# Kernel tuning notes

Measured on AMD Instinct MI355X. Metric: run time of the kernel, lower is better.

The kernel has to match this reference:

```python
import jax, jax.numpy as jnp
import numpy as np

EMBED = 1024
HEADS = 16
HDIM = EMBED // HEADS  # k_dim == v_dim == 64
MAXPOS = 256
L = 2 * MAXPOS  # rpe table length = 512
B, S = 1, 2048
EPS = 1e-6


def setup_inputs() -> dict:
    key = jax.random.key(0)
    ks = jax.random.split(key, 16)
    def xavier(k, shape):
        fan_in, fan_out = shape[1], shape[0]
        std = (2.0 / (fan_in + fan_out)) ** 0.5
        return jax.random.normal(k, shape, dtype=jnp.float32) * std
    inp = {
        "query": jax.random.normal(ks[0], (B, S, EMBED), dtype=jnp.float32),
        "key":   jax.random.normal(ks[1], (B, S, EMBED), dtype=jnp.float32),
        "value": jax.random.normal(ks[2], (B, S, EMBED), dtype=jnp.float32),
        "pos":   jax.random.randint(ks[3], (B, S, S), 0, L, dtype=jnp.int32),
        "mask":  jnp.ones((B, S, S), dtype=jnp.float32),
        # projections (stored as [out, in] like torch Linear)
        "Wq": xavier(ks[4], (HEADS * HDIM, EMBED)), "bq": jnp.zeros((HEADS * HDIM,), jnp.float32),
        "Wk": xavier(ks[5], (HEADS * HDIM, EMBED)), "bk": jnp.zeros((HEADS * HDIM,), jnp.float32),
        "Wv": xavier(ks[6], (HEADS * HDIM, EMBED)), "bv": jnp.zeros((HEADS * HDIM,), jnp.float32),
        "rpe": jnp.zeros((L, HEADS, HDIM), jnp.float32) + 0.02 * jax.random.normal(ks[7], (L, HEADS, HDIM), dtype=jnp.float32),
        "Wqt": xavier(ks[8], (EMBED, EMBED)), "bqt": jnp.zeros((EMBED,), jnp.float32),
        "Wo": xavier(ks[9], (EMBED, HEADS * HDIM)), "bo": jnp.zeros((EMBED,), jnp.float32),
        "gamma": jnp.ones((EMBED,), jnp.float32),
        "beta": jnp.zeros((EMBED,), jnp.float32),
    }
    return inp


def _layer_norm(x, gamma, beta):
    mu = jnp.mean(x, axis=-1, keepdims=True)
    var = jnp.mean(jnp.square(x - mu), axis=-1, keepdims=True)
    return (x - mu) * jax.lax.rsqrt(var + EPS) * gamma + beta


def reference(query, key, value, pos, mask, Wq, bq, Wk, bk, Wv, bv, rpe, Wqt, bqt, Wo, bo, gamma, beta):
    b, s, _ = query.shape
    scaling = HDIM ** (-0.5)
    q = (query @ Wq.T + bq) * scaling          # [b,s,n*d]
    k = key @ Wk.T + bk
    v = value @ Wv.T + bv
    q = q.reshape(b, s, HEADS, HDIM)
    k = k.reshape(b, s, HEADS, HDIM)
    v = v.reshape(b, s, HEADS, HDIM)
    attn = jnp.einsum('bqnd,bknd->bqkn', q, k)          # [b,q,k,n]
    qrpe = jnp.einsum('bqnd,lnd->bqln', q, rpe)         # [b,q,L,n]
    idx = jnp.broadcast_to(pos[..., None], (b, s, s, HEADS))
    qrpe_g = jnp.take_along_axis(qrpe, idx, axis=2)     # gather per (q,k) pair
    attn = attn + qrpe_g
    attn = attn - (1.0 - mask[..., None]) * 1e6
    attn = jax.nn.softmax(attn, axis=-2)                # softmax over key axis
    out = jnp.einsum('bqkn,bknd->bqnd', attn, v).reshape(b, s, HEADS * HDIM)
    out = (out @ Wo.T + bo) + (query @ Wqt.T + bqt)
    return _layer_norm(out, gamma, beta)
```

## Files before the change

kernel.cpp:

```cpp
#include <hip/hip_runtime.h>


typedef short          bf16x8 __attribute__((ext_vector_type(8)));
typedef float          f32x4  __attribute__((ext_vector_type(4)));
typedef int            i32x4  __attribute__((ext_vector_type(4)));
typedef unsigned short u16x4  __attribute__((ext_vector_type(4)));
typedef unsigned short u16x8  __attribute__((ext_vector_type(8)));

#define SEQ 2048
#define EMB 1024
#define NH  16
#define HD  64
#define RL  512

#define MFMA16(a,b,c) __builtin_amdgcn_mfma_f32_16x16x32_bf16((a),(b),(c),0,0,0)

__device__ __forceinline__ unsigned short f2bf(float f){
  union{float f; unsigned u;} x; x.f=f;
  unsigned r = x.u + 0x7FFFu + ((x.u>>16)&1u);
  return (unsigned short)(r>>16);
}
__device__ __forceinline__ float bf2f(unsigned short u){
  union{unsigned u; float f;} x; x.u=((unsigned)u)<<16; return x.f;
}
__device__ __forceinline__ unsigned char f2e5(float f){
  union{_Float16 h; unsigned short u;} cv; cv.h = (_Float16)f;
  unsigned short b = cv.u;
  unsigned r = (unsigned)b + 0x7Fu + ((b>>8)&1u);
  return (unsigned char)(r>>8);
}
__device__ __forceinline__ float e52f(unsigned char b){
  union{unsigned short u; _Float16 h;} cv; cv.u = ((unsigned short)b)<<8;
  return (float)cv.h;
}
__device__ __forceinline__ void gload16(const void* g, void* l){
  __builtin_amdgcn_global_load_lds((const __attribute__((address_space(1))) unsigned int*)g,
                                   (__attribute__((address_space(3))) unsigned int*)l, 16, 0, 0);
}
__device__ __forceinline__ bf16x8 fragld(const unsigned short* t, int row, int chunk){
  int swz = chunk ^ (row & 7);
  return *(const bf16x8*)(t + row*64 + swz*8);
}

__global__ __launch_bounds__(256) void cvt_all(
    const float* __restrict__ s0, const float* __restrict__ s1, const float* __restrict__ s2,
    const float* __restrict__ s3, const float* __restrict__ s4, const float* __restrict__ s5,
    const float* __restrict__ s6, const float* __restrict__ s7,
    unsigned short* __restrict__ d0, unsigned short* __restrict__ d1, unsigned short* __restrict__ d2,
    unsigned short* __restrict__ d3, unsigned short* __restrict__ d4, unsigned short* __restrict__ d5,
    unsigned short* __restrict__ d6, unsigned short* __restrict__ d7)
{
  const float* s; unsigned short* d; int n;
  switch (blockIdx.y) {
    case 0: s=s0; d=d0; n=SEQ*EMB; break;
    case 1: s=s1; d=d1; n=SEQ*EMB; break;
    case 2: s=s2; d=d2; n=SEQ*EMB; break;
    case 3: s=s3; d=d3; n=EMB*EMB; break;
    case 4: s=s4; d=d4; n=EMB*EMB; break;
    case 5: s=s5; d=d5; n=EMB*EMB; break;
    case 6: s=s6; d=d6; n=EMB*EMB; break;
    default: s=s7; d=d7; n=EMB*EMB; break;
  }
  int i = (blockIdx.x*256 + threadIdx.x)*8;
  if (i >= n) return;
  f32x4 a = *(const f32x4*)(s+i);
  f32x4 b = *(const f32x4*)(s+i+4);
  u16x8 o;
  #pragma unroll
  for (int j=0;j<4;++j){ o[j]=f2bf(a[j]); o[4+j]=f2bf(b[j]); }
  *(u16x8*)(d+i) = o;
}

__global__ __launch_bounds__(256) void rpe_cvt(const float* __restrict__ src,
                                               unsigned short* __restrict__ dst)
{
  int i = (blockIdx.x*256 + threadIdx.x)*4;
  int l = i >> 10;
  int h = (i >> 6) & 15;
  int d = i & 63;
  f32x4 a = *(const f32x4*)(src + i);
  u16x4 o;
  #pragma unroll
  for (int j=0;j<4;++j) o[j]=f2bf(a[j]);
  *(u16x4*)(dst + ((size_t)h*RL + l)*HD + d) = o;
}

__global__ __launch_bounds__(256) void pack_pm(const int* __restrict__ pos,
                                               const float* __restrict__ mask,
                                               unsigned short* __restrict__ pm)
{
  int i = (blockIdx.x*256 + threadIdx.x)*4;
  i32x4 p = *(const i32x4*)(pos + i);
  f32x4 m = *(const f32x4*)(mask + i);
  u16x4 o;
  #pragma unroll
  for (int j=0;j<4;++j) o[j] = (m[j] > 0.5f) ? (unsigned short)p[j] : (unsigned short)512;
  *(u16x4*)(pm + i) = o;
}

__device__ __forceinline__ void gemm_core(const unsigned short* __restrict__ A,
                                          const unsigned short* __restrict__ W,
                                          unsigned short* At, unsigned short* Wt,
                                          f32x4 acc[4][4], int m0, int n0)
{
  const int tid = threadIdx.x, lane = tid & 63, w = tid >> 6;
  const int rg = lane >> 3, sc = (lane & 7) ^ rg;
  const int c = lane & 15, g = lane >> 4;
  const int wm = w >> 1, wn = w & 1;

  for (int kt = 0; kt < EMB/64; ++kt) {
    __syncthreads();
    #pragma unroll
    for (int i = 0; i < 4; ++i) {
      int r = w*32 + i*8 + rg;
      gload16(A + (size_t)(m0+r)*EMB + kt*64 + sc*8, At + (w*32 + i*8)*64);
      gload16(W + (size_t)(n0+r)*EMB + kt*64 + sc*8, Wt + (w*32 + i*8)*64);
    }
    __syncthreads();
    #pragma unroll
    for (int kk = 0; kk < 2; ++kk) {
      bf16x8 af[4], bw[4];
      #pragma unroll
      for (int mf = 0; mf < 4; ++mf) af[mf] = fragld(At, wm*64 + mf*16 + c, kk*4 + g);
      #pragma unroll
      for (int nf = 0; nf < 4; ++nf) bw[nf] = fragld(Wt, wn*64 + nf*16 + c, kk*4 + g);
      #pragma unroll
      for (int mf = 0; mf < 4; ++mf)
        #pragma unroll
        for (int nf = 0; nf < 4; ++nf)
          acc[mf][nf] = MFMA16(af[mf], bw[nf], acc[mf][nf]);
    }
  }
}

__global__ __launch_bounds__(256) void gemm_proj(
    const unsigned short* __restrict__ Aq, const unsigned short* __restrict__ Ak,
    const unsigned short* __restrict__ Av,
    const unsigned short* __restrict__ Wq, const unsigned short* __restrict__ Wk,
    const unsigned short* __restrict__ Wv, const unsigned short* __restrict__ Wqt,
    const float* __restrict__ bq, const float* __restrict__ bk,
    const float* __restrict__ bv, const float* __restrict__ bqt,
    unsigned short* __restrict__ q_out, unsigned short* __restrict__ k_out,
    unsigned short* __restrict__ vt_out, float* __restrict__ qt_out)
{
  __shared__ alignas(16) unsigned short At[128*64];
  __shared__ alignas(16) unsigned short Wt[128*64];
  const unsigned short *A, *W; const float* bias;
  const int z = blockIdx.z;
  if      (z == 0) { A=Aq; W=Wq;  bias=bq;  }
  else if (z == 1) { A=Ak; W=Wk;  bias=bk;  }
  else if (z == 2) { A=Av; W=Wv;  bias=bv;  }
  else             { A=Aq; W=Wqt; bias=bqt; }

  f32x4 acc[4][4];
  #pragma unroll
  for (int i=0;i<4;++i)
    #pragma unroll
    for (int j=0;j<4;++j) acc[i][j] = (f32x4){0.f,0.f,0.f,0.f};

  const int m0 = blockIdx.y*128, n0 = blockIdx.x*128;
  gemm_core(A, W, At, Wt, acc, m0, n0);

  const int lane = threadIdx.x & 63, w = threadIdx.x >> 6;
  const int c = lane & 15, g = lane >> 4, wm = w >> 1, wn = w & 1;
  const float QSCALE = 0.125f * 1.4426950408889634f;
  #pragma unroll
  for (int nf = 0; nf < 4; ++nf) {
    int n = n0 + wn*64 + nf*16 + c;
    float b = bias[n];
    #pragma unroll
    for (int mf = 0; mf < 4; ++mf) {
      int mb = m0 + wm*64 + mf*16 + g*4;
      if (z == 0) {
        #pragma unroll
        for (int j=0;j<4;++j) q_out[(size_t)(mb+j)*EMB + n] = f2bf((acc[mf][nf][j] + b)*QSCALE);
      } else if (z == 1) {
        #pragma unroll
        for (int j=0;j<4;++j) k_out[(size_t)(mb+j)*EMB + n] = f2bf(acc[mf][nf][j] + b);
      } else if (z == 2) {
        u16x4 pk;
        #pragma unroll
        for (int j=0;j<4;++j) pk[j] = f2bf(acc[mf][nf][j] + b);
        *(u16x4*)(vt_out + (size_t)n*SEQ + mb) = pk;
      } else {
        #pragma unroll
        for (int j=0;j<4;++j) qt_out[(size_t)(mb+j)*EMB + n] = acc[mf][nf][j] + b;
      }
    }
  }
}

__global__ __launch_bounds__(256) void gemm_wo(
    const unsigned short* __restrict__ A, const unsigned short* __restrict__ W,
    const float* __restrict__ bo, float* __restrict__ qt)
{
  __shared__ alignas(16) unsigned short At[128*64];
  __shared__ alignas(16) unsigned short Wt[128*64];
  f32x4 acc[4][4];
  #pragma unroll
  for (int i=0;i<4;++i)
    #pragma unroll
    for (int j=0;j<4;++j) acc[i][j] = (f32x4){0.f,0.f,0.f,0.f};
  const int m0 = blockIdx.y*128, n0 = blockIdx.x*128;
  gemm_core(A, W, At, Wt, acc, m0, n0);

  const int lane = threadIdx.x & 63, w = threadIdx.x >> 6;
  const int c = lane & 15, g = lane >> 4, wm = w >> 1, wn = w & 1;
  #pragma unroll
  for (int nf = 0; nf < 4; ++nf) {
    int n = n0 + wn*64 + nf*16 + c;
    float b = bo[n];
    #pragma unroll
    for (int mf = 0; mf < 4; ++mf) {
      int mb = m0 + wm*64 + mf*16 + g*4;
      #pragma unroll
      for (int j=0;j<4;++j) {
        size_t idx = (size_t)(mb+j)*EMB + n;
        qt[idx] = acc[mf][nf][j] + b + qt[idx];
      }
    }
  }
}

__global__ __launch_bounds__(256) void attn_kernel(
    const unsigned short* __restrict__ q_bf, const unsigned short* __restrict__ k_bf,
    const unsigned short* __restrict__ vt_bf, const unsigned short* __restrict__ rpe_bf,
    const unsigned short* __restrict__ pm, unsigned short* __restrict__ att_out)
{
  __shared__ alignas(16) unsigned char pool[38144];
  unsigned short* k_tile  = (unsigned short*)(pool);
  unsigned short* vt_tile = (unsigned short*)(pool + 8192);
  unsigned char*  table8  = pool + 16384;
  unsigned short* q_tile  = (unsigned short*)(pool + 33024);
  unsigned short* p_base  = (unsigned short*)(pool + 33024);
  float*          red     = (float*)(pool);
  float*          red2    = (float*)(pool + 33024);

  const int tid = threadIdx.x, lane = tid & 63, w = tid >> 6;
  const int qh = w & 1, ks = w >> 1;
  const int h = blockIdx.y;
  const int q0 = blockIdx.x * 32;
  const int rg = lane >> 3, sc = (lane & 7) ^ rg;
  const int c = lane & 15, g = lane >> 4;

  gload16(q_bf + (size_t)(q0 + w*8 + rg)*EMB + h*HD + sc*8, q_tile + (w*8)*64);
  __syncthreads();

  for (int ch = 0; ch < 8; ++ch) {
    __syncthreads();
    #pragma unroll
    for (int i = 0; i < 2; ++i)
      gload16(rpe_bf + ((size_t)h*RL + ch*64 + w*16 + i*8 + rg)*HD + sc*8,
              k_tile + (w*16 + i*8)*64);
    __syncthreads();
    #pragma unroll
    for (int qq = 0; qq < 2; ++qq) {
      f32x4 dd = (f32x4){0.f,0.f,0.f,0.f};
      dd = MFMA16(fragld(k_tile, w*16 + c, g),     fragld(q_tile, qq*16 + c, g),     dd);
      dd = MFMA16(fragld(k_tile, w*16 + c, 4 + g), fragld(q_tile, qq*16 + c, 4 + g), dd);
      unsigned pk = (unsigned)f2e5(dd[0]) | ((unsigned)f2e5(dd[1])<<8)
                  | ((unsigned)f2e5(dd[2])<<16) | ((unsigned)f2e5(dd[3])<<24);
      *(unsigned*)(table8 + (qq*16 + c)*520 + ch*64 + w*16 + g*4) = pk;
    }
  }
  if (tid < 32) table8[tid*520 + 512] = 0xFC;

  f32x4 oacc[4];
  #pragma unroll
  for (int i=0;i<4;++i) oacc[i] = (f32x4){0.f,0.f,0.f,0.f};
  float sump = 0.f;
  const bf16x8 qf0 = fragld(q_tile, qh*16 + c, g);
  const bf16x8 qf1 = fragld(q_tile, qh*16 + c, 4 + g);
  unsigned short* pw = p_base + w*640;
  const unsigned char* trow = table8 + (qh*16 + c)*520;
  const size_t qg = (size_t)(q0 + qh*16 + c)*SEQ;

  for (int kt = 0; kt < SEQ/64; ++kt) {
    const int kb = kt*64;
    __syncthreads();
    #pragma unroll
    for (int i = 0; i < 2; ++i) {
      gload16(k_bf  + (size_t)(kb + w*16 + i*8 + rg)*EMB + h*HD + sc*8, k_tile  + (w*16 + i*8)*64);
      gload16(vt_bf + ((size_t)h*HD + w*16 + i*8 + rg)*SEQ + kb + sc*8, vt_tile + (w*16 + i*8)*64);
    }
    u16x4 pv0 = *(const u16x4*)(pm + qg + kb + ks*32 + g*4);
    u16x4 pv1 = *(const u16x4*)(pm + qg + kb + ks*32 + 16 + g*4);
    __syncthreads();

    #pragma unroll
    for (int kf = 0; kf < 2; ++kf) {
      f32x4 sf = (f32x4){0.f,0.f,0.f,0.f};
      sf = MFMA16(fragld(k_tile, ks*32 + kf*16 + c, g),     qf0, sf);
      sf = MFMA16(fragld(k_tile, ks*32 + kf*16 + c, 4 + g), qf1, sf);
      u16x4 pv = kf ? pv1 : pv0;
      u16x4 pk;
      #pragma unroll
      for (int j = 0; j < 4; ++j) {
        float rv = e52f(trow[pv[j]]);
        float p  = exp2f(sf[j] + rv);
        sump += p;
        pk[j] = f2bf(p);
      }
      *(u16x4*)(pw + c*40 + kf*16 + g*4) = pk;
    }
    asm volatile("s_waitcnt lgkmcnt(0)" ::: "memory");
    bf16x8 pa = *(const bf16x8*)(pw + c*40 + g*8);
    #pragma unroll
    for (int df = 0; df < 4; ++df)
      oacc[df] = MFMA16(pa, fragld(vt_tile, df*16 + c, ks*4 + g), oacc[df]);
  }

  sump += __shfl_xor(sump, 16);
  sump += __shfl_xor(sump, 32);

  __syncthreads();
  if (ks) {
    #pragma unroll
    for (int df = 0; df < 4; ++df)
      *(f32x4*)(&red[(qh*64 + lane)*16 + df*4]) = oacc[df];
    if (g == 0) red2[qh*16 + c] = sump;
  }
  __syncthreads();
  if (!ks) {
    sump += red2[qh*16 + c];
    #pragma unroll
    for (int df = 0; df < 4; ++df)
      oacc[df] += *(const f32x4*)(&red[(qh*64 + lane)*16 + df*4]);
    #pragma unroll
    for (int j = 0; j < 4; ++j) {
      float inv = 1.0f / __shfl(sump, g*4 + j);
      int qrow = q0 + qh*16 + g*4 + j;
      #pragma unroll
      for (int df = 0; df < 4; ++df)
        att_out[(size_t)qrow*EMB + h*HD + df*16 + c] = f2bf(oacc[df][j] * inv);
    }
  }
}

__global__ __launch_bounds__(256) void ln_kernel(const float* __restrict__ x,
                                                 const float* __restrict__ gamma,
                                                 const float* __restrict__ beta,
                                                 float* __restrict__ out)
{
  const int row = blockIdx.x, t = threadIdx.x;
  f32x4 v = *(const f32x4*)(x + (size_t)row*EMB + t*4);
  float s = v[0]+v[1]+v[2]+v[3];
  #pragma unroll
  for (int o = 32; o > 0; o >>= 1) s += __shfl_xor(s, o);
  __shared__ float r1[4], r2[4];
  if ((t & 63) == 0) r1[t >> 6] = s;
  __syncthreads();
  float mean = (r1[0]+r1[1]+r1[2]+r1[3]) * (1.0f/EMB);
  f32x4 d; float q = 0.f;
  #pragma unroll
  for (int j=0;j<4;++j){ d[j] = v[j] - mean; q += d[j]*d[j]; }
  #pragma unroll
  for (int o = 32; o > 0; o >>= 1) q += __shfl_xor(q, o);
  if ((t & 63) == 0) r2[t >> 6] = q;
  __syncthreads();
  float var = (r2[0]+r2[1]+r2[2]+r2[3]) * (1.0f/EMB);
  float rs = rsqrtf(var + 1e-6f);
  f32x4 gg = *(const f32x4*)(gamma + t*4);
  f32x4 bb = *(const f32x4*)(beta  + t*4);
  f32x4 o4;
  #pragma unroll
  for (int j=0;j<4;++j) o4[j] = d[j]*rs*gg[j] + bb[j];
  *(f32x4*)(out + (size_t)row*EMB + t*4) = o4;
}

extern "C" void kernel_launch(void* const* d_in, const int* in_sizes, int n_in,
                              void* d_out, int out_size, void* d_ws, size_t ws_size,
                              hipStream_t stream)
{
  (void)in_sizes; (void)n_in; (void)out_size;
  const float* query = (const float*)d_in[0];
  const float* key   = (const float*)d_in[1];
  const float* value = (const float*)d_in[2];
  const int*   pos   = (const int*)  d_in[3];
  const float* mask  = (const float*)d_in[4];
  const float* Wq    = (const float*)d_in[5];
  const float* bq    = (const float*)d_in[6];
  const float* Wk    = (const float*)d_in[7];
  const float* bk    = (const float*)d_in[8];
  const float* Wv    = (const float*)d_in[9];
  const float* bv    = (const float*)d_in[10];
  const float* rpe   = (const float*)d_in[11];
  const float* Wqt   = (const float*)d_in[12];
  const float* bqt   = (const float*)d_in[13];
  const float* Wo    = (const float*)d_in[14];
  const float* bo    = (const float*)d_in[15];
  const float* gamma = (const float*)d_in[16];
  const float* beta  = (const float*)d_in[17];
  float* out = (float*)d_out;

  char* ws = (char*)d_ws;
  const size_t OFF_QBF   = 0;
  const size_t OFF_KBF   = 4194304;
  const size_t OFF_VTBF  = 8388608;
  const size_t OFF_QRYBF = 12582912;
  const size_t OFF_KEYBF = 16777216;
  const size_t OFF_VALBF = 20971520;
  const size_t OFF_WQ    = 25165824;
  const size_t OFF_WK    = 27262976;
  const size_t OFF_WV    = 29360128;
  const size_t OFF_WQT   = 31457280;
  const size_t OFF_WO    = 33554432;
  const size_t OFF_RPE   = 35651584;
  const size_t OFF_QT    = 36700160;
  const size_t OFF_ATT   = 45088768;
  const size_t WS_NEED   = 49283072;
  if (ws_size < WS_NEED) return;

  unsigned short* q_bf   = (unsigned short*)(ws + OFF_QBF);
  unsigned short* k_bf   = (unsigned short*)(ws + OFF_KBF);
  unsigned short* vt_bf  = (unsigned short*)(ws + OFF_VTBF);
  unsigned short* qry_bf = (unsigned short*)(ws + OFF_QRYBF);
  unsigned short* key_bf = (unsigned short*)(ws + OFF_KEYBF);
  unsigned short* val_bf = (unsigned short*)(ws + OFF_VALBF);
  unsigned short* wq_bf  = (unsigned short*)(ws + OFF_WQ);
  unsigned short* wk_bf  = (unsigned short*)(ws + OFF_WK);
  unsigned short* wv_bf  = (unsigned short*)(ws + OFF_WV);
  unsigned short* wqt_bf = (unsigned short*)(ws + OFF_WQT);
  unsigned short* wo_bf  = (unsigned short*)(ws + OFF_WO);
  unsigned short* rpe_bf = (unsigned short*)(ws + OFF_RPE);
  float*          qt     = (float*)         (ws + OFF_QT);
  unsigned short* att_bf = (unsigned short*)(ws + OFF_ATT);
  unsigned short* pm16   = (unsigned short*)(ws + OFF_QRYBF);

  cvt_all<<<dim3(1024, 8), 256, 0, stream>>>(
      query, key, value, Wq, Wk, Wv, Wqt, Wo,
      qry_bf, key_bf, val_bf, wq_bf, wk_bf, wv_bf, wqt_bf, wo_bf);
  rpe_cvt<<<512, 256, 0, stream>>>(rpe, rpe_bf);
  gemm_proj<<<dim3(8, 16, 4), 256, 0, stream>>>(
      qry_bf, key_bf, val_bf, wq_bf, wk_bf, wv_bf, wqt_bf,
      bq, bk, bv, bqt, q_bf, k_bf, vt_bf, qt);
  pack_pm<<<SEQ*SEQ/1024, 256, 0, stream>>>(pos, mask, pm16);
  attn_kernel<<<dim3(SEQ/32, NH), 256, 0, stream>>>(
      q_bf, k_bf, vt_bf, rpe_bf, pm16, att_bf);
  gemm_wo<<<dim3(8, 16), 256, 0, stream>>>(att_bf, wo_bf, bo, qt);
  ln_kernel<<<2048, 256, 0, stream>>>(qt, gamma, beta, out);
}
```

Before: 146.3 us.

## Fuse rpe conversion, prefetch packed mask, compute softmax sum via MFMA

Folds the rpe conversion into the bulk conversion kernel, which removes one launch. pack_pm now writes pos/mask in a permuted layout so each lane loads 8 contiguous indices, and the next tile's indices are prefetched. In the attention inner loop, exp2f is replaced with raw v_exp_f32, the bf16 conversions use the packed v_cvt_pk_bf16_f32 instruction, and the row sum is computed by an extra MFMA against a ones vector instead of scalar adds and shuffles. s_setprio hints are added around the MFMA blocks in the GEMMs and attention. The risks are lower exp precision, since no denormal handling is done, and summing bf16-rounded probabilities for the normaliser.

```diff
diff --git a/kernel.cpp b/kernel.cpp
--- a/kernel.cpp
+++ b/kernel.cpp
@@ -6,6 +6,7 @@
 typedef int            i32x4  __attribute__((ext_vector_type(4)));
 typedef unsigned short u16x4  __attribute__((ext_vector_type(4)));
 typedef unsigned short u16x8  __attribute__((ext_vector_type(8)));
+typedef unsigned int   u32x2  __attribute__((ext_vector_type(2)));
 
 #define SEQ 2048
 #define EMB 1024
@@ -20,8 +21,13 @@
   unsigned r = x.u + 0x7FFFu + ((x.u>>16)&1u);
   return (unsigned short)(r>>16);
 }
-__device__ __forceinline__ float bf2f(unsigned short u){
-  union{unsigned u; float f;} x; x.u=((unsigned)u)<<16; return x.f;
+__device__ __forceinline__ unsigned cvtpk(float a, float b){
+  unsigned r;
+  asm("v_cvt_pk_bf16_f32 %0, %1, %2" : "=v"(r) : "v"(a), "v"(b));
+  return r;
+}
+__device__ __forceinline__ float fexp2(float x){
+  float r; asm("v_exp_f32 %0, %1" : "=v"(r) : "v"(x)); return r;
 }
 __device__ __forceinline__ unsigned char f2e5(float f){
   union{_Float16 h; unsigned short u;} cv; cv.h = (_Float16)f;
@@ -29,8 +35,8 @@
   unsigned r = (unsigned)b + 0x7Fu + ((b>>8)&1u);
   return (unsigned char)(r>>8);
 }
-__device__ __forceinline__ float e52f(unsigned char b){
-  union{unsigned short u; _Float16 h;} cv; cv.u = ((unsigned short)b)<<8;
+__device__ __forceinline__ float e52f(unsigned short b){
+  union{unsigned short u; _Float16 h;} cv; cv.u = (unsigned short)(b<<8);
   return (float)cv.h;
 }
 __device__ __forceinline__ void gload16(const void* g, void* l){
@@ -48,8 +54,20 @@
     const float* __restrict__ s6, const float* __restrict__ s7,
     unsigned short* __restrict__ d0, unsigned short* __restrict__ d1, unsigned short* __restrict__ d2,
     unsigned short* __restrict__ d3, unsigned short* __restrict__ d4, unsigned short* __restrict__ d5,
-    unsigned short* __restrict__ d6, unsigned short* __restrict__ d7)
-{
+    unsigned short* __restrict__ d6, unsigned short* __restrict__ d7,
+    const float* __restrict__ rpe, unsigned short* __restrict__ rpe_bf)
+{
+  if (blockIdx.y == 8) {
+    int i = (blockIdx.x*256 + threadIdx.x)*4;
+    if (i >= RL*NH*HD) return;
+    int l = i >> 10, h = (i >> 6) & 15, d = i & 63;
+    f32x4 a = *(const f32x4*)(rpe + i);
+    u16x4 o;
+    #pragma unroll
+    for (int j=0;j<4;++j) o[j]=f2bf(a[j]);
+    *(u16x4*)(rpe_bf + ((size_t)h*RL + l)*HD + d) = o;
+    return;
+  }
   const float* s; unsigned short* d; int n;
   switch (blockIdx.y) {
     case 0: s=s0; d=d0; n=SEQ*EMB; break;
@@ -71,31 +89,25 @@
   *(u16x8*)(d+i) = o;
 }
 
-__global__ __launch_bounds__(256) void rpe_cvt(const float* __restrict__ src,
-                                               unsigned short* __restrict__ dst)
-{
-  int i = (blockIdx.x*256 + threadIdx.x)*4;
-  int l = i >> 10;
-  int h = (i >> 6) & 15;
-  int d = i & 63;
-  f32x4 a = *(const f32x4*)(src + i);
-  u16x4 o;
-  #pragma unroll
-  for (int j=0;j<4;++j) o[j]=f2bf(a[j]);
-  *(u16x4*)(dst + ((size_t)h*RL + l)*HD + d) = o;
-}
-
 __global__ __launch_bounds__(256) void pack_pm(const int* __restrict__ pos,
                                                const float* __restrict__ mask,
                                                unsigned short* __restrict__ pm)
 {
-  int i = (blockIdx.x*256 + threadIdx.x)*4;
-  i32x4 p = *(const i32x4*)(pos + i);
-  f32x4 m = *(const f32x4*)(mask + i);
-  u16x4 o;
-  #pragma unroll
-  for (int j=0;j<4;++j) o[j] = (m[j] > 0.5f) ? (unsigned short)p[j] : (unsigned short)512;
-  *(u16x4*)(pm + i) = o;
+  int i = (blockIdx.x*256 + threadIdx.x)*8;
+  i32x4 p0 = *(const i32x4*)(pos + i);
+  i32x4 p1 = *(const i32x4*)(pos + i + 4);
+  f32x4 m0 = *(const f32x4*)(mask + i);
+  f32x4 m1 = *(const f32x4*)(mask + i + 4);
+  u16x4 lo, hi;
+  #pragma unroll
+  for (int j=0;j<4;++j){
+    lo[j] = (m0[j] > 0.5f) ? (unsigned short)p0[j] : (unsigned short)512;
+    hi[j] = (m1[j] > 0.5f) ? (unsigned short)p1[j] : (unsigned short)512;
+  }
+  int grp = i & ~31;
+  int o0  = ((i & 15) >> 2)*8 + ((i >> 4) & 1)*4;
+  *(u16x4*)(pm + grp + o0)     = lo;
+  *(u16x4*)(pm + grp + o0 + 8) = hi;
 }
 
 __device__ __forceinline__ void gemm_core(const unsigned short* __restrict__ A,
@@ -124,11 +136,13 @@
       for (int mf = 0; mf < 4; ++mf) af[mf] = fragld(At, wm*64 + mf*16 + c, kk*4 + g);
       #pragma unroll
       for (int nf = 0; nf < 4; ++nf) bw[nf] = fragld(Wt, wn*64 + nf*16 + c, kk*4 + g);
+      __builtin_amdgcn_s_setprio(1);
       #pragma unroll
       for (int mf = 0; mf < 4; ++mf)
         #pragma unroll
         for (int nf = 0; nf < 4; ++nf)
           acc[mf][nf] = MFMA16(af[mf], bw[nf], acc[mf][nf]);
+      __builtin_amdgcn_s_setprio(0);
     }
   }
 }
@@ -234,7 +248,7 @@
   unsigned short* q_tile  = (unsigned short*)(pool + 33024);
   unsigned short* p_base  = (unsigned short*)(pool + 33024);
   float*          red     = (float*)(pool);
-  float*          red2    = (float*)(pool + 33024);
+  float*          red2    = (float*)(pool + 8192);
 
   const int tid = threadIdx.x, lane = tid & 63, w = tid >> 6;
   const int qh = w & 1, ks = w >> 1;
@@ -242,6 +256,7 @@
   const int q0 = blockIdx.x * 32;
   const int rg = lane >> 3, sc = (lane & 7) ^ rg;
   const int c = lane & 15, g = lane >> 4;
+  const bf16x8 kOnes = {16256,16256,16256,16256,16256,16256,16256,16256};
 
   gload16(q_bf + (size_t)(q0 + w*8 + rg)*EMB + h*HD + sc*8, q_tile + (w*8)*64);
   __syncthreads();
@@ -268,12 +283,14 @@
   f32x4 oacc[4];
   #pragma unroll
   for (int i=0;i<4;++i) oacc[i] = (f32x4){0.f,0.f,0.f,0.f};
-  float sump = 0.f;
+  f32x4 osum = (f32x4){0.f,0.f,0.f,0.f};
   const bf16x8 qf0 = fragld(q_tile, qh*16 + c, g);
   const bf16x8 qf1 = fragld(q_tile, qh*16 + c, 4 + g);
   unsigned short* pw = p_base + w*640;
   const unsigned char* trow = table8 + (qh*16 + c)*520;
-  const size_t qg = (size_t)(q0 + qh*16 + c)*SEQ;
+  const unsigned short* pmrow = pm + (size_t)(q0 + qh*16 + c)*SEQ + ks*32 + g*8;
+
+  u16x8 pvv = *(const u16x8*)(pmrow);
 
   for (int kt = 0; kt < SEQ/64; ++kt) {
     const int kb = kt*64;
@@ -283,52 +300,50 @@
       gload16(k_bf  + (size_t)(kb + w*16 + i*8 + rg)*EMB + h*HD + sc*8, k_tile  + (w*16 + i*8)*64);
       gload16(vt_bf + ((size_t)h*HD + w*16 + i*8 + rg)*SEQ + kb + sc*8, vt_tile + (w*16 + i*8)*64);
     }
-    u16x4 pv0 = *(const u16x4*)(pm + qg + kb + ks*32 + g*4);
-    u16x4 pv1 = *(const u16x4*)(pm + qg + kb + ks*32 + 16 + g*4);
+    u16x8 pvv_n = *(const u16x8*)(pmrow + ((kb + 64) & (SEQ-1)));
     __syncthreads();
 
     #pragma unroll
     for (int kf = 0; kf < 2; ++kf) {
       f32x4 sf = (f32x4){0.f,0.f,0.f,0.f};
+      __builtin_amdgcn_s_setprio(1);
       sf = MFMA16(fragld(k_tile, ks*32 + kf*16 + c, g),     qf0, sf);
       sf = MFMA16(fragld(k_tile, ks*32 + kf*16 + c, 4 + g), qf1, sf);
-      u16x4 pv = kf ? pv1 : pv0;
-      u16x4 pk;
-      #pragma unroll
-      for (int j = 0; j < 4; ++j) {
-        float rv = e52f(trow[pv[j]]);
-        float p  = exp2f(sf[j] + rv);
-        sump += p;
-        pk[j] = f2bf(p);
-      }
-      *(u16x4*)(pw + c*40 + kf*16 + g*4) = pk;
-    }
+      __builtin_amdgcn_s_setprio(0);
+      float p0 = fexp2(sf[0] + e52f(trow[pvv[kf*4+0]]));
+      float p1 = fexp2(sf[1] + e52f(trow[pvv[kf*4+1]]));
+      float p2 = fexp2(sf[2] + e52f(trow[pvv[kf*4+2]]));
+      float p3 = fexp2(sf[3] + e52f(trow[pvv[kf*4+3]]));
+      u32x2 pk; pk[0] = cvtpk(p0, p1); pk[1] = cvtpk(p2, p3);
+      *(u32x2*)(pw + c*40 + kf*16 + g*4) = pk;
+    }
+    pvv = pvv_n;
     asm volatile("s_waitcnt lgkmcnt(0)" ::: "memory");
     bf16x8 pa = *(const bf16x8*)(pw + c*40 + g*8);
+    __builtin_amdgcn_s_setprio(1);
     #pragma unroll
     for (int df = 0; df < 4; ++df)
       oacc[df] = MFMA16(pa, fragld(vt_tile, df*16 + c, ks*4 + g), oacc[df]);
-  }
-
-  sump += __shfl_xor(sump, 16);
-  sump += __shfl_xor(sump, 32);
+    osum = MFMA16(pa, kOnes, osum);
+    __builtin_amdgcn_s_setprio(0);
+  }
 
   __syncthreads();
   if (ks) {
     #pragma unroll
     for (int df = 0; df < 4; ++df)
       *(f32x4*)(&red[(qh*64 + lane)*16 + df*4]) = oacc[df];
-    if (g == 0) red2[qh*16 + c] = sump;
+    if (c == 0) *(f32x4*)(&red2[(qh*4 + g)*4]) = osum;
   }
   __syncthreads();
   if (!ks) {
-    sump += red2[qh*16 + c];
+    osum += *(const f32x4*)(&red2[(qh*4 + g)*4]);
     #pragma unroll
     for (int df = 0; df < 4; ++df)
       oacc[df] += *(const f32x4*)(&red[(qh*64 + lane)*16 + df*4]);
     #pragma unroll
     for (int j = 0; j < 4; ++j) {
-      float inv = 1.0f / __shfl(sump, g*4 + j);
+      float inv = 1.0f / osum[j];
       int qrow = q0 + qh*16 + g*4 + j;
       #pragma unroll
       for (int df = 0; df < 4; ++df)
@@ -427,14 +442,14 @@
   unsigned short* att_bf = (unsigned short*)(ws + OFF_ATT);
   unsigned short* pm16   = (unsigned short*)(ws + OFF_QRYBF);
 
-  cvt_all<<<dim3(1024, 8), 256, 0, stream>>>(
+  cvt_all<<<dim3(1024, 9), 256, 0, stream>>>(
       query, key, value, Wq, Wk, Wv, Wqt, Wo,
-      qry_bf, key_bf, val_bf, wq_bf, wk_bf, wv_bf, wqt_bf, wo_bf);
-  rpe_cvt<<<512, 256, 0, stream>>>(rpe, rpe_bf);
+      qry_bf, key_bf, val_bf, wq_bf, wk_bf, wv_bf, wqt_bf, wo_bf,
+      rpe, rpe_bf);
   gemm_proj<<<dim3(8, 16, 4), 256, 0, stream>>>(
       qry_bf, key_bf, val_bf, wq_bf, wk_bf, wv_bf, wqt_bf,
       bq, bk, bv, bqt, q_bf, k_bf, vt_bf, qt);
-  pack_pm<<<SEQ*SEQ/1024, 256, 0, stream>>>(pos, mask, pm16);
+  pack_pm<<<SEQ*SEQ/2048, 256, 0, stream>>>(pos, mask, pm16);
   attn_kernel<<<dim3(SEQ/32, NH), 256, 0, stream>>>(
       q_bf, k_bf, vt_bf, rpe_bf, pm16, att_bf);
   gemm_wo<<<dim3(8, 16), 256, 0, stream>>>(att_bf, wo_bf, bo, qt);
```

Result: faster. 128.2 us (-12.4%).
